# Kernel optimization log

Hardware: AMD Instinct MI355X
Metric: run time of the kernel (lower is better)

The kernel has to match this reference:

```python
import jax, jax.numpy as jnp
import numpy as np

LENGTH = 100
EMBED = 64
BATCH = 8192


def setup_inputs() -> dict:
    key = jax.random.key(0)
    k1, k2 = jax.random.split(key)
    x = jax.random.normal(k1, (BATCH, LENGTH), dtype=jnp.float32)
    # learned embedding table (nn.Embedding weight)
    W = jax.random.normal(k2, (LENGTH, EMBED), dtype=jnp.float32)
    return {"x": x, "W": W}


def reference(x, W):
    # Torch module computes: result[b, 0, i*E + j] = x[b, i] * W[i, j]
    # (the sparse selector matmul `x @ trans` merely repeats each x column E times,
    #  and the tiled embedding lookup flattens W per batch row).
    B, L = x.shape
    E = W.shape[1]
    out = x[:, :, None] * W[None, :, :]          # [B, L, E]
    return out.reshape(B, 1, L * E)
```

## Files before the change

### kernel.cpp

```cpp
#include <hip/hip_runtime.h>
#include <hip/hip_bf16.h>


#define LENGTH 100
#define EMBED 64
#define BATCH 8192
#define V4_PER_ROW (LENGTH * EMBED / 4)
#define TPB 320

typedef float vfloat4 __attribute__((ext_vector_type(4)));

__global__ __launch_bounds__(TPB) void chemical_embedding_kernel(
    const float* __restrict__ x,
    const float* __restrict__ W,
    float* __restrict__ out)
{
    const int b = blockIdx.x;
    const int t = threadIdx.x;

    const vfloat4* __restrict__ W4 = reinterpret_cast<const vfloat4*>(W);
    const float*   __restrict__ xrow = x + b * LENGTH;
    vfloat4*       __restrict__ orow = reinterpret_cast<vfloat4*>(out) + b * V4_PER_ROW;

#pragma unroll
    for (int k = 0; k < V4_PER_ROW / TPB; ++k) {
        const int r = k * TPB + t;
        const float s = xrow[r >> 4];
        vfloat4 w = W4[r];
        vfloat4 o = s * w;
        __builtin_nontemporal_store(o, &orow[r]);
    }
}

extern "C" void kernel_launch(void* const* d_in, const int* in_sizes, int n_in,
                              void* d_out, int out_size, void* d_ws, size_t ws_size,
                              hipStream_t stream) {
    const float* x = (const float*)d_in[0];
    const float* W = (const float*)d_in[1];
    float* out = (float*)d_out;

    chemical_embedding_kernel<<<BATCH, TPB, 0, stream>>>(x, W, out);
}
```

Before: 222.4 us.

## Hold W slice in registers and loop over batch slices per thread

Restructures the grid into column slices by batch slices so that each thread loads its W vec4 once and reuses it across 32 batch rows at a fixed stride. This removes repeated W loads and index math per output element and changes the per-thread work pattern. It also drops the nontemporal store hint in favour of regular stores, which may change how the large output stream interacts with the caches.

```diff
diff --git a/kernel.cpp b/kernel.cpp
--- a/kernel.cpp
+++ b/kernel.cpp
@@ -7,6 +7,7 @@
 #define BATCH 8192
 #define V4_PER_ROW (LENGTH * EMBED / 4)
 #define TPB 320
+#define BSLICES 256
 
 typedef float vfloat4 __attribute__((ext_vector_type(4)));
 
@@ -15,20 +16,25 @@
     const float* __restrict__ W,
     float* __restrict__ out)
 {
-    const int b = blockIdx.x;
-    const int t = threadIdx.x;
+    const int r = blockIdx.x * TPB + threadIdx.x;
+    const int i = r >> 4;
 
-    const vfloat4* __restrict__ W4 = reinterpret_cast<const vfloat4*>(W);
-    const float*   __restrict__ xrow = x + b * LENGTH;
-    vfloat4*       __restrict__ orow = reinterpret_cast<vfloat4*>(out) + b * V4_PER_ROW;
+    const vfloat4 w = reinterpret_cast<const vfloat4*>(W)[r];
 
-#pragma unroll
-    for (int k = 0; k < V4_PER_ROW / TPB; ++k) {
-        const int r = k * TPB + t;
-        const float s = xrow[r >> 4];
-        vfloat4 w = W4[r];
-        vfloat4 o = s * w;
-        __builtin_nontemporal_store(o, &orow[r]);
+    const int b0 = blockIdx.y;
+    const float* __restrict__ xp = x + b0 * LENGTH + i;
+    vfloat4* __restrict__ op =
+        reinterpret_cast<vfloat4*>(out) + (size_t)b0 * V4_PER_ROW + r;
+
+    const int xstep = BSLICES * LENGTH;
+    const int ostep = BSLICES * V4_PER_ROW;
+
+#pragma unroll 4
+    for (int it = 0; it < BATCH / BSLICES; ++it) {
+        const float s = *xp;
+        *op = s * w;
+        xp += xstep;
+        op += ostep;
     }
 }
 
@@ -39,5 +45,6 @@
     const float* W = (const float*)d_in[1];
     float* out = (float*)d_out;
 
-    chemical_embedding_kernel<<<BATCH, TPB, 0, stream>>>(x, W, out);
+    dim3 grid(V4_PER_ROW / TPB, BSLICES);
+    chemical_embedding_kernel<<<grid, TPB, 0, stream>>>(x, W, out);
 }
```

Measured after the change: 205.5 us. 7.6% less time.
